# Kernel tuning notes

Measured on AMD Instinct MI355X. Metric: run time of the kernel, lower is better.

## Reference

```python
import jax, jax.numpy as jnp
import numpy as np

HID, FFN, E, K = 1024, 4096, 8, 2
CAP_FACTOR = 1.25


def setup_inputs() -> dict:
    key = jax.random.key(0)
    k1, k2, k3, k4 = jax.random.split(key, 4)
    B, T = 4, 2048
    x = jax.random.normal(k1, (B, T, HID), dtype=jnp.float32)
    router_w = jax.random.normal(k2, (E, HID), dtype=jnp.float32) * 0.02
    w1 = jax.random.normal(k3, (E, HID, FFN), dtype=jnp.float32) * 0.02
    w2 = jax.random.normal(k4, (E, FFN, HID), dtype=jnp.float32) * 0.02
    return {"x": x, "router_w": router_w, "w1": w1, "w2": w2}


def reference(x, router_w, w1, w2):
    B, T, H = x.shape
    N = B * T
    x_flat = x.reshape(N, H)
    # capacity per expert (static, shape-derived)
    C = max(1, int(CAP_FACTOR * N / E * K))

    # router (eval mode: no noise)
    logits = x_flat @ router_w.T                      # [N, E]
    probs = jax.nn.softmax(logits, axis=-1)
    top_v, top_i = jax.lax.top_k(probs, K)            # [N, K]
    top_v = top_v / jnp.sum(top_v, axis=-1, keepdims=True)

    out = jnp.zeros_like(x_flat)
    for k in range(K):
        eid = top_i[:, k]                             # [N] expert id per token
        gate = top_v[:, k]                            # [N]
        # position of each token within its expert, in token order
        onehot = jax.nn.one_hot(eid, E, dtype=jnp.int32)          # [N, E]
        pos = jnp.take_along_axis(jnp.cumsum(onehot, axis=0), eid[:, None], axis=1)[:, 0] - 1
        keep = pos < C                                # capacity drop (first C in token order)
        slot = jnp.where(keep, eid * C + pos, E * C)  # dropped tokens -> dump slot

        # dispatch: scatter kept tokens into per-expert capacity buffers
        buf = jnp.zeros((E * C + 1, H), dtype=x.dtype).at[slot].add(
            x_flat * keep[:, None].astype(x.dtype))
        expert_in = buf[: E * C].reshape(E, C, H)     # [E, C, H]

        # per-expert FFN (grouped GEMM -> GELU -> grouped GEMM)
        h = jax.nn.gelu(jnp.einsum('ech,ehf->ecf', expert_in, w1), approximate=False)
        y = jnp.einsum('ecf,efh->ech', h, w2)         # [E, C, H]

        # combine: gather back to token order, mask dropped, apply gate
        tok = y.reshape(E * C, H)[jnp.minimum(slot, E * C - 1)]
        out = out + tok * (gate * keep.astype(x.dtype))[:, None]

    return out.reshape(B, T, H)
```

## Files before the change

### kernel.cpp

```cpp
#include <hip/hip_runtime.h>
#include <hip/hip_bf16.h>
#include <math.h>

#define N_TOK 8192
#define HIDD  1024
#define FFND  4096
#define NE    8
#define CAP   2560
#define TMX   20
#define RMAX  16512
#define PBLK  128

typedef __attribute__((ext_vector_type(4)))  float  f32x4;
typedef __attribute__((ext_vector_type(16))) float  f32x16;
typedef __attribute__((ext_vector_type(8)))  __bf16 bf16x8;

__device__ __forceinline__ unsigned short f2bf(float f) {
    unsigned u = __float_as_uint(f);
    u = (u + 0x7fffu + ((u >> 16) & 1u)) >> 16;
    return (unsigned short)u;
}

__device__ __forceinline__ float gelu_f(float v) {
    float x  = v * 0.70710678118654752f;
    float ax = fabsf(x);
    float t  = 1.0f / (1.0f + 0.3275911f * ax);
    float poly = ((((1.061405429f * t - 1.453152027f) * t + 1.421413741f) * t
                   - 0.284496736f) * t + 0.254829592f) * t;
    float er = 1.0f - poly * __expf(-x * x);
    er = copysignf(er, x);
    return 0.5f * v * (1.0f + er);
}

__device__ __forceinline__ void gld_lds16(const void* g, void* l) {
    __builtin_amdgcn_global_load_lds(
        (const __attribute__((address_space(1))) unsigned int*)g,
        (__attribute__((address_space(3))) unsigned int*)l, 16, 0, 0);
}

__global__ __launch_bounds__(256) void transpose_cvt2(const float* __restrict__ W1,
                                                      const float* __restrict__ W2,
                                                      unsigned short* __restrict__ W1t,
                                                      unsigned short* __restrict__ W2t) {
    __shared__ unsigned short st[64][72];
    int z = blockIdx.z;
    int R = (z < NE) ? HIDD : FFND;
    int C = (z < NE) ? FFND : HIDD;
    int e = (z < NE) ? z : z - NE;
    if (blockIdx.x >= (unsigned)(C / 64) || blockIdx.y >= (unsigned)(R / 64)) return;
    const float* W = (z < NE) ? W1 : W2;
    unsigned short* Wt = (z < NE) ? W1t : W2t;

    int r0 = blockIdx.y * 64, c0 = blockIdx.x * 64;
    int tid = threadIdx.x;
    int rb = tid >> 4, cq = tid & 15;
    const float* src = W + ((size_t)e * R + r0) * C + c0;
#pragma unroll
    for (int i = 0; i < 4; i++) {
        int kr = i * 16 + rb;
        float4 v = *reinterpret_cast<const float4*>(src + (size_t)kr * C + cq * 4);
        st[cq * 4 + 0][kr] = f2bf(v.x);
        st[cq * 4 + 1][kr] = f2bf(v.y);
        st[cq * 4 + 2][kr] = f2bf(v.z);
        st[cq * 4 + 3][kr] = f2bf(v.w);
    }
    __syncthreads();
    unsigned short* dst = Wt + ((size_t)e * C + c0) * R + r0;
#pragma unroll
    for (int i = 0; i < 4; i++) {
        int cr = i * 16 + rb;
        uint2 v = *reinterpret_cast<const uint2*>(&st[cr][cq * 4]);
        *reinterpret_cast<uint2*>(dst + (size_t)cr * R + cq * 4) = v;
    }
}

__global__ __launch_bounds__(256) void router_kernel(const float* __restrict__ x,
                                                     const float* __restrict__ rw,
                                                     unsigned short* __restrict__ xbf,
                                                     int* __restrict__ cnt,
                                                     int* __restrict__ tok,
                                                     float* __restrict__ gate) {
    __shared__ float4 rwl[2048];
    __shared__ int   e0s[32], e1s[32];
    __shared__ float g0s[32], g1s[32];
    __shared__ int   baseS[16];

    int tid = threadIdx.x, lane = tid & 63, w = tid >> 6;
    for (int i = tid; i < 2048; i += 256) rwl[i] = reinterpret_cast<const float4*>(rw)[i];
    __syncthreads();

    int tbase = blockIdx.x * 32 + w * 8;
    for (int i = 0; i < 8; i++) {
        int t = tbase + i;
        const float4* xr = reinterpret_cast<const float4*>(x) + (size_t)t * 256;
        float4 xv[4];
#pragma unroll
        for (int c = 0; c < 4; c++) xv[c] = xr[c * 64 + lane];
        uint2* xb = reinterpret_cast<uint2*>(xbf) + (size_t)t * 256;
#pragma unroll
        for (int c = 0; c < 4; c++) {
            uint2 p;
            p.x = (unsigned)f2bf(xv[c].x) | ((unsigned)f2bf(xv[c].y) << 16);
            p.y = (unsigned)f2bf(xv[c].z) | ((unsigned)f2bf(xv[c].w) << 16);
            xb[c * 64 + lane] = p;
        }
        float dot[NE];
#pragma unroll
        for (int e = 0; e < NE; e++) {
            float s = 0.f;
#pragma unroll
            for (int c = 0; c < 4; c++) {
                float4 a = rwl[e * 256 + c * 64 + lane];
                s += xv[c].x * a.x + xv[c].y * a.y + xv[c].z * a.z + xv[c].w * a.w;
            }
            dot[e] = s;
        }
#pragma unroll
        for (int e = 0; e < NE; e++) {
            float v = dot[e];
#pragma unroll
            for (int o = 32; o > 0; o >>= 1) v += __shfl_xor(v, o, 64);
            dot[e] = v;
        }
        if (lane == 0) {
            int e0 = 0; float l0 = dot[0];
#pragma unroll
            for (int e = 1; e < NE; e++) if (dot[e] > l0) { l0 = dot[e]; e0 = e; }
            int e1 = -1; float l1 = -3.4e38f;
#pragma unroll
            for (int e = 0; e < NE; e++) if (e != e0 && dot[e] > l1) { l1 = dot[e]; e1 = e; }
            float g0 = 1.f / (1.f + expf(l1 - l0));
            int j = w * 8 + i;
            e0s[j] = e0; e1s[j] = e1; g0s[j] = g0; g1s[j] = 1.f - g0;
        }
    }
    __syncthreads();

    int e0 = 255, e1 = 255, rank0 = 0, rank1 = 0, slotcnt = 0;
    float g0 = 0.f, g1 = 0.f;
    if (w == 0) {
        if (lane < 32) { e0 = e0s[lane]; e1 = e1s[lane]; g0 = g0s[lane]; g1 = g1s[lane]; }
        unsigned long long lt = (1ull << lane) - 1ull;
#pragma unroll
        for (int ee = 0; ee < NE; ee++) {
            unsigned long long m0 = __ballot(e0 == ee);
            unsigned long long m1 = __ballot(e1 == ee);
            if (e0 == ee) rank0 = (int)__popcll(m0 & lt);
            if (e1 == ee) rank1 = (int)__popcll(m1 & lt);
            if (lane == ee)      slotcnt = (int)__popcll(m0);
            if (lane == NE + ee) slotcnt = (int)__popcll(m1);
        }
        if (lane < 16) baseS[lane] = atomicAdd(&cnt[lane * 16], slotcnt);
    }
    __syncthreads();
    if (w == 0 && lane < 32) {
        int t = blockIdx.x * 32 + lane;
        int p0 = baseS[e0] + rank0;
        if (p0 < CAP) { tok[e0 * CAP + p0] = t; gate[e0 * CAP + p0] = g0; }
        int p1 = baseS[NE + e1] + rank1;
        if (p1 < CAP) { tok[(NE + e1) * CAP + p1] = t; gate[(NE + e1) * CAP + p1] = g1; }
    }
}

template <int KD, int ND, int KS, int CH, bool G1F>
__global__ __launch_bounds__(256, 4) void ffn_gemm_q(const unsigned short* __restrict__ A,
                                                     const unsigned short* __restrict__ Bw,
                                                     unsigned short* __restrict__ H,
                                                     float* __restrict__ O,
                                                     const int* __restrict__ cntAll,
                                                     const int* __restrict__ tokL,
                                                     const float* __restrict__ gateL) {
    constexpr int TN    = ND / 128;
    constexpr int UNITS = TN * KS;
    constexpr int KDS   = KD / KS;

    __shared__ __align__(16) unsigned short At[128 * 64];
    __shared__ __align__(16) unsigned short Bt[128 * 64];

    int e  = blockIdx.x & 7;
    int pb = blockIdx.x >> 3;

    int cnt0 = min(cntAll[e * 16], CAP);
    int cnt1 = min(cntAll[(e + 8) * 16], CAP);
    int tmx0 = (cnt0 + 127) >> 7, tmx1 = (cnt1 + 127) >> 7;
    int tmsum = tmx0 + tmx1;
    if (tmsum == 0) return;
    int per_chunk = tmsum * CH;
    int total = tmsum * UNITS;

    int offA = 0, offB = 0;
#pragma unroll
    for (int t = 0; t < 16; t++) {
        int cc = min(cntAll[t * 16], CAP);
        if (t < e)     offA += cc;
        if (t < e + 8) offB += cc;
    }

    int tid = threadIdx.x;
    int w = tid >> 6, l = tid & 63;
    int wr = w >> 1, wc = w & 1;

    int sr  = tid >> 3;
    int ssw = (((tid & 7) ^ ((tid >> 4) & 7)) << 4);
    char* aD[4];
    char* bD[4];
#pragma unroll
    for (int j = 0; j < 4; j++) {
        aD[j] = (char*)At + j * 4096 + w * 1024;
        bD[j] = (char*)Bt + j * 4096 + w * 1024;
    }

    int l31 = l & 31, hi = l >> 5;
    int s8  = (l31 >> 1) & 7;
    int kt[4];
#pragma unroll
    for (int kh = 0; kh < 4; kh++) kt[kh] = (((kh * 2 + hi) ^ s8) << 4);
    int aRdB[2], bRdB[2];
#pragma unroll
    for (int mi = 0; mi < 2; mi++) {
        aRdB[mi] = (wr * 64 + mi * 32 + l31) * 128;
        bRdB[mi] = (wc * 64 + mi * 32 + l31) * 128;
    }

    for (int u0 = pb; u0 < total; u0 += PBLK) {
        int c = u0 / per_chunk;
        int r = u0 - c * per_chunk;
        int s, tm, cnt_e, off_e;
        if (r < tmx0 * CH) { s = e;     tm = r / CH; r -= tm * CH; cnt_e = cnt0; off_e = offA; }
        else { r -= tmx0 * CH; s = e + 8; tm = r / CH; r -= tm * CH; cnt_e = cnt1; off_e = offB; }
        int u  = c * CH + r;
        int tn = (KS > 1) ? (u / KS) : u;
        int ks = (KS > 1) ? (u % KS) : 0;
        const int lbase = s * CAP;

        const char* aS[4];
        const char* bS[4];
#pragma unroll
        for (int j = 0; j < 4; j++) {
            int p = tm * 128 + j * 32 + sr;
            int rowg;
            if (G1F) rowg = tokL[lbase + (p < cnt_e ? p : 0)];
            else     rowg = off_e + p;
            aS[j] = (const char*)(A + (size_t)rowg * KD + ks * KDS) + ssw;
            bS[j] = (const char*)(Bw + ((size_t)e * ND + tn * 128 + j * 32 + sr) * KD + ks * KDS) + ssw;
        }

        f32x16 a00, a01, a10, a11;
#pragma unroll
        for (int i = 0; i < 16; i++) { a00[i] = 0.f; a01[i] = 0.f; a10[i] = 0.f; a11[i] = 0.f; }

        for (int k0 = 0; k0 < KDS; k0 += 64) {
            size_t kb = (size_t)k0 * 2;
#pragma unroll
            for (int j = 0; j < 4; j++) gld_lds16(aS[j] + kb, aD[j]);
#pragma unroll
            for (int j = 0; j < 4; j++) gld_lds16(bS[j] + kb, bD[j]);
            __syncthreads();
            const char* Atc = (const char*)At;
            const char* Btc = (const char*)Bt;
            __builtin_amdgcn_s_setprio(1);
#pragma unroll
            for (int kh = 0; kh < 4; kh++) {
                bf16x8 fa0 = *reinterpret_cast<const bf16x8*>(Atc + aRdB[0] + kt[kh]);
                bf16x8 fa1 = *reinterpret_cast<const bf16x8*>(Atc + aRdB[1] + kt[kh]);
                bf16x8 fb0 = *reinterpret_cast<const bf16x8*>(Btc + bRdB[0] + kt[kh]);
                bf16x8 fb1 = *reinterpret_cast<const bf16x8*>(Btc + bRdB[1] + kt[kh]);
                a00 = __builtin_amdgcn_mfma_f32_32x32x16_bf16(fa0, fb0, a00, 0, 0, 0);
                a01 = __builtin_amdgcn_mfma_f32_32x32x16_bf16(fa0, fb1, a01, 0, 0, 0);
                a10 = __builtin_amdgcn_mfma_f32_32x32x16_bf16(fa1, fb0, a10, 0, 0, 0);
                a11 = __builtin_amdgcn_mfma_f32_32x32x16_bf16(fa1, fb1, a11, 0, 0, 0);
            }
            __builtin_amdgcn_s_setprio(0);
            __syncthreads();
        }

#pragma unroll
        for (int mi = 0; mi < 2; mi++) {
#pragma unroll
            for (int reg = 0; reg < 16; reg++) {
                int rr = wr * 64 + mi * 32 + (reg & 3) + 8 * (reg >> 2) + 4 * hi;
                int p  = tm * 128 + rr;
                if (p < cnt_e) {
                    float v0 = (mi == 0) ? a00[reg] : a10[reg];
                    float v1 = (mi == 0) ? a01[reg] : a11[reg];
                    if (G1F) {
                        unsigned short* hp = H + (size_t)(off_e + p) * ND + tn * 128 + wc * 64 + l31;
                        hp[0]  = f2bf(gelu_f(v0));
                        hp[32] = f2bf(gelu_f(v1));
                    } else {
                        int t = tokL[lbase + p];
                        float gv = gateL[lbase + p];
                        float* op = O + (size_t)t * ND + tn * 128 + wc * 64 + l31;
                        atomicAdd(op,      gv * v0);
                        atomicAdd(op + 32, gv * v1);
                    }
                }
            }
        }
    }
}

template <int KD, int ND, bool G1>
__global__ __launch_bounds__(256) void ffn_gemm(const unsigned short* __restrict__ A,
                                                const float* __restrict__ W,
                                                unsigned short* __restrict__ H,
                                                float* __restrict__ O,
                                                const int* __restrict__ cntAll,
                                                const int* __restrict__ tokL,
                                                const float* __restrict__ gateL,
                                                int slot0, int pbase) {
    constexpr int TN = ND / 128;
    int bid = blockIdx.x;
    int tn  = bid % TN;
    int tme = bid / TN;
    int tm  = tme % TMX;
    int s   = slot0 + tme / TMX;
    int eW  = s & 7;
    int cnt_e = min(cntAll[s * 16], CAP);
    if (tm * 128 >= cnt_e) return;
    int off_e = 0;
#pragma unroll
    for (int i = 0; i < 16; i++) {
        int c = min(cntAll[i * 16], CAP);
        off_e += (i >= pbase && i < s) ? c : 0;
    }
    const int lbase = s * CAP;

    __shared__ __align__(16) unsigned short At[128 * 32];
    __shared__ __align__(16) unsigned short Bt[128 * 32];

    int tid = threadIdx.x;
    int w = tid >> 6, l = tid & 63;
    int wr = w >> 1, wc = w & 1;

    int r1 = tid >> 2, q1 = tid & 3;
    int r2 = r1 + 64;
    const char* aSrc1;
    const char* aSrc2;
    if (G1) {
        int p1 = tm * 128 + r1, p2 = tm * 128 + r2;
        int t1 = tokL[lbase + (p1 < cnt_e ? p1 : 0)];
        int t2 = tokL[lbase + (p2 < cnt_e ? p2 : 0)];
        aSrc1 = (const char*)(A + (size_t)t1 * KD) + ((q1 ^ ((r1 >> 1) & 3)) << 4);
        aSrc2 = (const char*)(A + (size_t)t2 * KD) + ((q1 ^ ((r2 >> 1) & 3)) << 4);
    } else {
        size_t row1 = (size_t)off_e + tm * 128 + r1;
        size_t row2 = row1 + 64;
        aSrc1 = (const char*)(A + row1 * KD) + ((q1 ^ ((r1 >> 1) & 3)) << 4);
        aSrc2 = (const char*)(A + row2 * KD) + ((q1 ^ ((r2 >> 1) & 3)) << 4);
    }
    char* aDst1 = (char*)At + w * 1024;
    char* aDst2 = aDst1 + 4096;

    const float* bSrc[4];
    int bOff[16];
#pragma unroll
    for (int j = 0; j < 4; j++) {
        int fidx = j * 1024 + tid * 4;
        int kk = fidx >> 7, n = fidx & 127;
        bSrc[j] = W + (size_t)eW * KD * ND + (size_t)kk * ND + tn * 128 + n;
#pragma unroll
        for (int i = 0; i < 4; i++) {
            int nn = n + i;
            bOff[j * 4 + i] = nn * 64 + ((((kk >> 3) ^ ((nn >> 1) & 3))) << 4) + ((kk & 7) << 1);
        }
    }

    int aro[4], bro[4];
#pragma unroll
    for (int m = 0; m < 4; m++) {
        int rr = wr * 64 + m * 16 + (l & 15);
        aro[m] = rr * 64 + (((l >> 4) ^ ((rr >> 1) & 3)) << 4);
        int cc = wc * 64 + m * 16 + (l & 15);
        bro[m] = cc * 64 + (((l >> 4) ^ ((cc >> 1) & 3)) << 4);
    }

    f32x4 zf = {0.f, 0.f, 0.f, 0.f};
    f32x4 acc[4][4];
#pragma unroll
    for (int m = 0; m < 4; m++)
#pragma unroll
        for (int n = 0; n < 4; n++) acc[m][n] = zf;

    for (int k0 = 0; k0 < KD; k0 += 32) {
        gld_lds16(aSrc1 + (size_t)k0 * 2, aDst1);
        gld_lds16(aSrc2 + (size_t)k0 * 2, aDst2);
        float4 bv[4];
#pragma unroll
        for (int j = 0; j < 4; j++) bv[j] = *reinterpret_cast<const float4*>(bSrc[j] + (size_t)k0 * ND);
        char* btc = (char*)Bt;
#pragma unroll
        for (int j = 0; j < 4; j++) {
            *(unsigned short*)(btc + bOff[j * 4 + 0]) = f2bf(bv[j].x);
            *(unsigned short*)(btc + bOff[j * 4 + 1]) = f2bf(bv[j].y);
            *(unsigned short*)(btc + bOff[j * 4 + 2]) = f2bf(bv[j].z);
            *(unsigned short*)(btc + bOff[j * 4 + 3]) = f2bf(bv[j].w);
        }
        __syncthreads();
        bf16x8 af[4], bf[4];
#pragma unroll
        for (int m = 0; m < 4; m++) af[m] = *reinterpret_cast<const bf16x8*>((const char*)At + aro[m]);
#pragma unroll
        for (int n = 0; n < 4; n++) bf[n] = *reinterpret_cast<const bf16x8*>((const char*)Bt + bro[n]);
#pragma unroll
        for (int m = 0; m < 4; m++)
#pragma unroll
            for (int n = 0; n < 4; n++)
                acc[m][n] = __builtin_amdgcn_mfma_f32_16x16x32_bf16(af[m], bf[n], acc[m][n], 0, 0, 0);
        __syncthreads();
    }

    if (G1) {
#pragma unroll
        for (int m = 0; m < 4; m++) {
#pragma unroll
            for (int j = 0; j < 4; j++) {
                int rr = wr * 64 + m * 16 + (l >> 4) * 4 + j;
                int p = tm * 128 + rr;
                if (p < cnt_e) {
                    size_t row = (size_t)(off_e + p);
                    unsigned short* hp = H + row * ND + tn * 128 + wc * 64 + (l & 15);
#pragma unroll
                    for (int n = 0; n < 4; n++) hp[n * 16] = f2bf(gelu_f(acc[m][n][j]));
                }
            }
        }
    } else {
#pragma unroll
        for (int m = 0; m < 4; m++) {
#pragma unroll
            for (int j = 0; j < 4; j++) {
                int rr = wr * 64 + m * 16 + (l >> 4) * 4 + j;
                int p = tm * 128 + rr;
                if (p < cnt_e) {
                    int t = tokL[lbase + p];
                    float gv = gateL[lbase + p];
                    float* op = O + (size_t)t * ND + tn * 128 + wc * 64 + (l & 15);
#pragma unroll
                    for (int n = 0; n < 4; n++) atomicAdd(op + n * 16, gv * acc[m][n][j]);
                }
            }
        }
    }
}

extern "C" void kernel_launch(void* const* d_in, const int* in_sizes, int n_in,
                              void* d_out, int out_size, void* d_ws, size_t ws_size,
                              hipStream_t stream) {
    const float* x  = (const float*)d_in[0];
    const float* rw = (const float*)d_in[1];
    const float* w1 = (const float*)d_in[2];
    const float* w2 = (const float*)d_in[3];
    float* out = (float*)d_out;
    char* ws = (char*)d_ws;

    int*   cnt  = (int*)ws;
    int*   tok  = (int*)(ws + 4096);
    float* gate = (float*)(ws + 4096 + 16 * CAP * 4);
    unsigned short* xbf = (unsigned short*)(ws + (1 << 20));
    size_t hOff = (1 << 20) + (size_t)N_TOK * HIDD * 2;
    unsigned short* h = (unsigned short*)(ws + hOff);

    size_t w1tSz = (size_t)NE * HIDD * FFND * 2;
    size_t hBig = (size_t)RMAX * FFND * 2;
    size_t needBig = hOff + hBig + 2 * w1tSz;

    hipMemsetAsync(cnt, 0, 1024, stream);
    hipMemsetAsync(d_out, 0, (size_t)N_TOK * HIDD * 4, stream);

    hipLaunchKernelGGL(router_kernel, dim3(N_TOK / 32), dim3(256), 0, stream,
                       x, rw, xbf, cnt, tok, gate);

    if (ws_size >= needBig) {
        unsigned short* w1t = (unsigned short*)(ws + hOff + hBig);
        unsigned short* w2t = (unsigned short*)(ws + hOff + hBig + w1tSz);
        hipLaunchKernelGGL(transpose_cvt2, dim3(FFND / 64, FFND / 64, 2 * NE), dim3(256), 0, stream,
                           w1, w2, w1t, w2t);
        hipLaunchKernelGGL((ffn_gemm_q<HIDD, FFND, 1, 8, true>), dim3(8 * PBLK), dim3(256), 0, stream,
                           xbf, w1t, h, (float*)nullptr, cnt, tok, gate);
        hipLaunchKernelGGL((ffn_gemm_q<FFND, HIDD, 2, 4, false>), dim3(8 * PBLK), dim3(256), 0, stream,
                           h, w2t, (unsigned short*)nullptr, out, cnt, tok, gate);
    } else {
        for (int k = 0; k < 2; k++) {
            hipLaunchKernelGGL((ffn_gemm<HIDD, FFND, true>), dim3(8 * TMX * (FFND / 128)), dim3(256), 0, stream,
                               xbf, w1, h, (float*)nullptr, cnt, tok, gate, 8 * k, 8 * k);
            hipLaunchKernelGGL((ffn_gemm<FFND, HIDD, false>), dim3(8 * TMX * (HIDD / 128)), dim3(256), 0, stream,
                               h, w2, (unsigned short*)nullptr, out, cnt, tok, gate, 8 * k, 8 * k);
        }
    }
}
```

Baseline: 525.0 us.

## Widen expert GEMM tile N to 256 and halve persistent block count

The persistent grouped-GEMM kernel moves from a 128x128 to a 128x256 output tile, so each wave holds 2x4 MFMA accumulators and the B tile in LDS doubles. The number of persistent blocks per expert drops from 128 to 64, occupancy hint goes from 4 to 2, chunk sizes are halved, and the setprio hints are removed. The aim is more MFMA work per LDS load and less re-reading of A tiles. In exchange, register and LDS use per block rise and fewer waves are resident to hide load latency.

After: 587.8 us. 1.12x slower.

```diff
diff --git a/kernel.cpp b/kernel.cpp
--- a/kernel.cpp
+++ b/kernel.cpp
@@ -9,7 +9,7 @@
 #define CAP   2560
 #define TMX   20
 #define RMAX  16512
-#define PBLK  128
+#define PBLK  64
 
 typedef __attribute__((ext_vector_type(4)))  float  f32x4;
 typedef __attribute__((ext_vector_type(16))) float  f32x16;
@@ -163,19 +163,19 @@
 }
 
 template <int KD, int ND, int KS, int CH, bool G1F>
-__global__ __launch_bounds__(256, 4) void ffn_gemm_q(const unsigned short* __restrict__ A,
+__global__ __launch_bounds__(256, 2) void ffn_gemm_q(const unsigned short* __restrict__ A,
                                                      const unsigned short* __restrict__ Bw,
                                                      unsigned short* __restrict__ H,
                                                      float* __restrict__ O,
                                                      const int* __restrict__ cntAll,
                                                      const int* __restrict__ tokL,
                                                      const float* __restrict__ gateL) {
-    constexpr int TN    = ND / 128;
+    constexpr int TN    = ND / 256;
     constexpr int UNITS = TN * KS;
     constexpr int KDS   = KD / KS;
 
     __shared__ __align__(16) unsigned short At[128 * 64];
-    __shared__ __align__(16) unsigned short Bt[128 * 64];
+    __shared__ __align__(16) unsigned short Bt[256 * 64];
 
     int e  = blockIdx.x & 7;
     int pb = blockIdx.x >> 3;
@@ -203,24 +203,22 @@
     int sr  = tid >> 3;
     int ssw = (((tid & 7) ^ ((tid >> 4) & 7)) << 4);
     char* aD[4];
-    char* bD[4];
-#pragma unroll
-    for (int j = 0; j < 4; j++) {
-        aD[j] = (char*)At + j * 4096 + w * 1024;
-        bD[j] = (char*)Bt + j * 4096 + w * 1024;
-    }
+    char* bD[8];
+#pragma unroll
+    for (int j = 0; j < 4; j++) aD[j] = (char*)At + j * 4096 + w * 1024;
+#pragma unroll
+    for (int j = 0; j < 8; j++) bD[j] = (char*)Bt + j * 4096 + w * 1024;
 
     int l31 = l & 31, hi = l >> 5;
     int s8  = (l31 >> 1) & 7;
     int kt[4];
 #pragma unroll
     for (int kh = 0; kh < 4; kh++) kt[kh] = (((kh * 2 + hi) ^ s8) << 4);
-    int aRdB[2], bRdB[2];
-#pragma unroll
-    for (int mi = 0; mi < 2; mi++) {
-        aRdB[mi] = (wr * 64 + mi * 32 + l31) * 128;
-        bRdB[mi] = (wc * 64 + mi * 32 + l31) * 128;
-    }
+    int aRdB[2], bRdB[4];
+#pragma unroll
+    for (int mi = 0; mi < 2; mi++) aRdB[mi] = (wr * 64 + mi * 32 + l31) * 128;
+#pragma unroll
+    for (int ni = 0; ni < 4; ni++) bRdB[ni] = (wc * 128 + ni * 32 + l31) * 128;
 
     for (int u0 = pb; u0 < total; u0 += PBLK) {
         int c = u0 / per_chunk;
@@ -234,7 +232,7 @@
         const int lbase = s * CAP;
 
         const char* aS[4];
-        const char* bS[4];
+        const char* bS[8];
 #pragma unroll
         for (int j = 0; j < 4; j++) {
             int p = tm * 128 + j * 32 + sr;
@@ -242,35 +240,43 @@
             if (G1F) rowg = tokL[lbase + (p < cnt_e ? p : 0)];
             else     rowg = off_e + p;
             aS[j] = (const char*)(A + (size_t)rowg * KD + ks * KDS) + ssw;
-            bS[j] = (const char*)(Bw + ((size_t)e * ND + tn * 128 + j * 32 + sr) * KD + ks * KDS) + ssw;
-        }
-
-        f32x16 a00, a01, a10, a11;
-#pragma unroll
-        for (int i = 0; i < 16; i++) { a00[i] = 0.f; a01[i] = 0.f; a10[i] = 0.f; a11[i] = 0.f; }
+        }
+#pragma unroll
+        for (int j = 0; j < 8; j++)
+            bS[j] = (const char*)(Bw + ((size_t)e * ND + tn * 256 + j * 32 + sr) * KD + ks * KDS) + ssw;
+
+        f32x16 acc[2][4];
+#pragma unroll
+        for (int mi = 0; mi < 2; mi++)
+#pragma unroll
+            for (int ni = 0; ni < 4; ni++)
+#pragma unroll
+                for (int i = 0; i < 16; i++) acc[mi][ni][i] = 0.f;
 
         for (int k0 = 0; k0 < KDS; k0 += 64) {
             size_t kb = (size_t)k0 * 2;
 #pragma unroll
             for (int j = 0; j < 4; j++) gld_lds16(aS[j] + kb, aD[j]);
 #pragma unroll
-            for (int j = 0; j < 4; j++) gld_lds16(bS[j] + kb, bD[j]);
+            for (int j = 0; j < 8; j++) gld_lds16(bS[j] + kb, bD[j]);
             __syncthreads();
             const char* Atc = (const char*)At;
             const char* Btc = (const char*)Bt;
-            __builtin_amdgcn_s_setprio(1);
 #pragma unroll
             for (int kh = 0; kh < 4; kh++) {
-                bf16x8 fa0 = *reinterpret_cast<const bf16x8*>(Atc + aRdB[0] + kt[kh]);
-                bf16x8 fa1 = *reinterpret_cast<const bf16x8*>(Atc + aRdB[1] + kt[kh]);
-                bf16x8 fb0 = *reinterpret_cast<const bf16x8*>(Btc + bRdB[0] + kt[kh]);
-                bf16x8 fb1 = *reinterpret_cast<const bf16x8*>(Btc + bRdB[1] + kt[kh]);
-                a00 = __builtin_amdgcn_mfma_f32_32x32x16_bf16(fa0, fb0, a00, 0, 0, 0);
-                a01 = __builtin_amdgcn_mfma_f32_32x32x16_bf16(fa0, fb1, a01, 0, 0, 0);
-                a10 = __builtin_amdgcn_mfma_f32_32x32x16_bf16(fa1, fb0, a10, 0, 0, 0);
-                a11 = __builtin_amdgcn_mfma_f32_32x32x16_bf16(fa1, fb1, a11, 0, 0, 0);
+                bf16x8 fa[2], fb[4];
+#pragma unroll
+                for (int mi = 0; mi < 2; mi++)
+                    fa[mi] = *reinterpret_cast<const bf16x8*>(Atc + aRdB[mi] + kt[kh]);
+#pragma unroll
+                for (int ni = 0; ni < 4; ni++)
+                    fb[ni] = *reinterpret_cast<const bf16x8*>(Btc + bRdB[ni] + kt[kh]);
+#pragma unroll
+                for (int mi = 0; mi < 2; mi++)
+#pragma unroll
+                    for (int ni = 0; ni < 4; ni++)
+                        acc[mi][ni] = __builtin_amdgcn_mfma_f32_32x32x16_bf16(fa[mi], fb[ni], acc[mi][ni], 0, 0, 0);
             }
-            __builtin_amdgcn_s_setprio(0);
             __syncthreads();
         }
 
@@ -281,18 +287,16 @@
                 int rr = wr * 64 + mi * 32 + (reg & 3) + 8 * (reg >> 2) + 4 * hi;
                 int p  = tm * 128 + rr;
                 if (p < cnt_e) {
-                    float v0 = (mi == 0) ? a00[reg] : a10[reg];
-                    float v1 = (mi == 0) ? a01[reg] : a11[reg];
                     if (G1F) {
-                        unsigned short* hp = H + (size_t)(off_e + p) * ND + tn * 128 + wc * 64 + l31;
-                        hp[0]  = f2bf(gelu_f(v0));
-                        hp[32] = f2bf(gelu_f(v1));
+                        unsigned short* hp = H + (size_t)(off_e + p) * ND + tn * 256 + wc * 128 + l31;
+#pragma unroll
+                        for (int ni = 0; ni < 4; ni++) hp[ni * 32] = f2bf(gelu_f(acc[mi][ni][reg]));
                     } else {
                         int t = tokL[lbase + p];
                         float gv = gateL[lbase + p];
-                        float* op = O + (size_t)t * ND + tn * 128 + wc * 64 + l31;
-                        atomicAdd(op,      gv * v0);
-                        atomicAdd(op + 32, gv * v1);
+                        float* op = O + (size_t)t * ND + tn * 256 + wc * 128 + l31;
+#pragma unroll
+                        for (int ni = 0; ni < 4; ni++) atomicAdd(op + ni * 32, gv * acc[mi][ni][reg]);
                     }
                 }
             }
@@ -476,9 +480,9 @@
         unsigned short* w2t = (unsigned short*)(ws + hOff + hBig + w1tSz);
         hipLaunchKernelGGL(transpose_cvt2, dim3(FFND / 64, FFND / 64, 2 * NE), dim3(256), 0, stream,
                            w1, w2, w1t, w2t);
-        hipLaunchKernelGGL((ffn_gemm_q<HIDD, FFND, 1, 8, true>), dim3(8 * PBLK), dim3(256), 0, stream,
+        hipLaunchKernelGGL((ffn_gemm_q<HIDD, FFND, 1, 4, true>), dim3(8 * PBLK), dim3(256), 0, stream,
                            xbf, w1t, h, (float*)nullptr, cnt, tok, gate);
-        hipLaunchKernelGGL((ffn_gemm_q<FFND, HIDD, 2, 4, false>), dim3(8 * PBLK), dim3(256), 0, stream,
+        hipLaunchKernelGGL((ffn_gemm_q<FFND, HIDD, 2, 2, false>), dim3(8 * PBLK), dim3(256), 0, stream,
                            h, w2t, (unsigned short*)nullptr, out, cnt, tok, gate);
     } else {
         for (int k = 0; k < 2; k++) {
```
